# Kernel tuning notes

Hardware: AMD Instinct MI355X
Metric: run time of the kernel (lower is better)

Reference implementation:

```python
import jax, jax.numpy as jnp
import numpy as np

N = 1048576   # total nodes across batch
B = 128       # number of graphs
H = 128       # hidden_size
NEG_SLOPE = 0.01  # LeakyReLU default


def setup_inputs() -> dict:
    key = jax.random.key(0)
    k1, k2, k3, k4 = jax.random.split(key, 4)
    h = jax.random.normal(k1, (N, H), dtype=jnp.float32)
    attention_query = jax.random.normal(k2, (B, H), dtype=jnp.float32)
    w = jax.random.normal(k3, (2 * H,), dtype=jnp.float32) * (1.0 / np.sqrt(2 * H))
    segment_ids = jnp.sort(jax.random.randint(k4, (N,), 0, B, dtype=jnp.int32))
    return {"h": h, "attention_query": attention_query, "w": w, "segment_ids": segment_ids}


def reference(h, attention_query, w, segment_ids):
    # gate_nn(concat([h, q_rep])) = h @ w[:H] + q[seg] @ w[H:], then LeakyReLU
    w_h, w_q = w[:H], w[H:]
    q_score = attention_query @ w_q                      # [B]
    gate = h @ w_h + q_score[segment_ids]                # [N]
    gate = jnp.where(gate >= 0, gate, NEG_SLOPE * gate)  # LeakyReLU
    # segment softmax over nodes of each graph
    m = jax.ops.segment_max(gate, segment_ids, num_segments=B)   # [B]
    m = jnp.where(jnp.isfinite(m), m, 0.0)               # guard empty segments
    e = jnp.exp(gate - m[segment_ids])                   # [N]
    denom = jax.ops.segment_sum(e, segment_ids, num_segments=B)  # [B]
    alpha = e / jnp.maximum(denom, 1e-20)[segment_ids]   # [N]
    # feat_nn takes first half of concat => just h; weighted segment sum
    pooled = jax.ops.segment_sum(alpha[:, None] * h, segment_ids, num_segments=B)  # [B, H]
    return pooled
```

## Files before the change

kernel.cpp:

```cpp
#include <hip/hip_runtime.h>
#include <math.h>

#define N_ROWS 1048576
#define H 128
#define B 128
#define NEG_SLOPE 0.01f

#define GRID_MAIN 2048
#define ROWS_PB (N_ROWS / GRID_MAIN)
#define MAXP 256

__device__ __forceinline__ float dot4(float4 a, float4 b) {
    return a.x * b.x + a.y * b.y + a.z * b.z + a.w * b.w;
}

__global__ __launch_bounds__(256) void qs_init_kernel(const float* __restrict__ aq,
                                                      const float* __restrict__ w,
                                                      float* __restrict__ qs,
                                                      int* __restrict__ counter) {
    if (blockIdx.x == 0 && threadIdx.x < B) counter[threadIdx.x] = 0;
    const int lane = threadIdx.x & 63;
    const int wave = threadIdx.x >> 6;
    const int half = lane >> 5;
    const int hl   = lane & 31;
    const int b    = blockIdx.x * 8 + wave * 2 + half;
    float4 w4 = ((const float4*)(w + H))[hl];
    float4 a4 = ((const float4*)(aq + (long)b * H))[hl];
    float d = dot4(a4, w4);
    #pragma unroll
    for (int off = 1; off < 32; off <<= 1) d += __shfl_xor(d, off, 32);
    if (hl == 0) qs[b] = d;
}

__global__ __launch_bounds__(256) void main_kernel(const float* __restrict__ h,
                                                   const int* __restrict__ seg,
                                                   const float* __restrict__ w,
                                                   const float* __restrict__ qs,
                                                   int* __restrict__ counter,
                                                   float* __restrict__ pm,
                                                   float* __restrict__ pd,
                                                   float* __restrict__ pacc) {
    __shared__ float qs_s[B];
    if (threadIdx.x < B) qs_s[threadIdx.x] = qs[threadIdx.x];
    __syncthreads();

    const int lane = threadIdx.x & 63;
    const int wave = threadIdx.x >> 6;
    const int half = lane >> 5;
    const int hl   = lane & 31;
    const int hwid = wave * 2 + half;
    const long r0  = (long)blockIdx.x * ROWS_PB;

    float4 w4 = ((const float4*)w)[hl];

    const int sFirst = seg[r0];
    const int sLast  = seg[r0 + ROWS_PB - 1];

    if (sFirst == sLast) {
        const float qsv = qs_s[sFirst];
        float  m_run = -1e30f;
        float  d_run = 0.0f;
        float4 acc   = {0.0f, 0.0f, 0.0f, 0.0f};

        for (int it = 0; it < ROWS_PB / 32; ++it) {
            long base = r0 + (long)it * 32 + hwid * 4;
            const float4* hp = (const float4*)(h + base * H) + hl;
            float4 h0 = hp[0];
            float4 h1 = hp[32];
            float4 h2 = hp[64];
            float4 h3 = hp[96];

            float d0 = dot4(h0, w4), d1 = dot4(h1, w4);
            float d2 = dot4(h2, w4), d3 = dot4(h3, w4);

            float s0 = d0 + __shfl_xor(d0, 16, 32);
            float s1 = d1 + __shfl_xor(d1, 16, 32);
            float s2 = d2 + __shfl_xor(d2, 16, 32);
            float s3 = d3 + __shfl_xor(d3, 16, 32);
            float z01 = (hl & 16) ? s1 : s0;
            float z23 = (hl & 16) ? s3 : s2;
            float t01 = z01 + __shfl_xor(z01, 8, 32);
            float t23 = z23 + __shfl_xor(z23, 8, 32);
            float zz  = (hl & 8) ? t23 : t01;
            zz += __shfl_xor(zz, 4, 32);
            zz += __shfl_xor(zz, 2, 32);
            zz += __shfl_xor(zz, 1, 32);
            float g0 = __shfl(zz,  0, 32) + qsv;
            float g1 = __shfl(zz, 16, 32) + qsv;
            float g2 = __shfl(zz,  8, 32) + qsv;
            float g3 = __shfl(zz, 24, 32) + qsv;
            g0 = (g0 >= 0.0f) ? g0 : NEG_SLOPE * g0;
            g1 = (g1 >= 0.0f) ? g1 : NEG_SLOPE * g1;
            g2 = (g2 >= 0.0f) ? g2 : NEG_SLOPE * g2;
            g3 = (g3 >= 0.0f) ? g3 : NEG_SLOPE * g3;

            #pragma unroll
            for (int u = 0; u < 4; ++u) {
                float  g  = (u == 0) ? g0 : (u == 1) ? g1 : (u == 2) ? g2 : g3;
                float4 hv = (u == 0) ? h0 : (u == 1) ? h1 : (u == 2) ? h2 : h3;
                if (g <= m_run) {
                    float e = __expf(g - m_run);
                    acc.x += e * hv.x;
                    acc.y += e * hv.y;
                    acc.z += e * hv.z;
                    acc.w += e * hv.w;
                    d_run += e;
                } else {
                    float sc = __expf(m_run - g);
                    acc.x = acc.x * sc + hv.x;
                    acc.y = acc.y * sc + hv.y;
                    acc.z = acc.z * sc + hv.z;
                    acc.w = acc.w * sc + hv.w;
                    d_run = d_run * sc + 1.0f;
                    m_run = g;
                }
            }
        }
        float m_o = __shfl_xor(m_run, 32);
        float d_o = __shfl_xor(d_run, 32);
        float4 a_o;
        a_o.x = __shfl_xor(acc.x, 32);
        a_o.y = __shfl_xor(acc.y, 32);
        a_o.z = __shfl_xor(acc.z, 32);
        a_o.w = __shfl_xor(acc.w, 32);
        float M  = fmaxf(m_run, m_o);
        float ss = __expf(m_run - M);
        float so = __expf(m_o  - M);
        float4 am;
        am.x = acc.x * ss + a_o.x * so;
        am.y = acc.y * ss + a_o.y * so;
        am.z = acc.z * ss + a_o.z * so;
        am.w = acc.w * ss + a_o.w * so;
        float Dm = d_run * ss + d_o * so;

        int slot = 0;
        if (lane == 0) slot = atomicAdd(counter + sFirst, 1);
        slot = min(__shfl(slot, 0), MAXP - 1);
        long pbase = (long)sFirst * MAXP + slot;
        if (half == 0) ((float4*)(pacc + pbase * H))[hl] = am;
        if (lane == 0) { pm[pbase] = M; pd[pbase] = Dm; }
    } else {
        int    cur   = -1;
        float  m_run = -1e30f;
        float  d_run = 0.0f;
        float4 acc   = {0.0f, 0.0f, 0.0f, 0.0f};

        for (int it = 0; it < ROWS_PB / 16; ++it) {
            long r1 = r0 + hwid + (long)it * 16;
            long r2 = r1 + 8;
            float4 ha = ((const float4*)(h + r1 * H))[hl];
            float4 hb = ((const float4*)(h + r2 * H))[hl];
            int s1 = seg[r1];
            int s2 = seg[r2];

            #pragma unroll
            for (int k = 0; k < 2; ++k) {
                float4 h4 = k ? hb : ha;
                int    s  = k ? s2 : s1;
                float d = dot4(h4, w4);
                #pragma unroll
                for (int off = 1; off < 32; off <<= 1) d += __shfl_xor(d, off, 32);
                float g = d + qs_s[s];
                g = (g >= 0.0f) ? g : NEG_SLOPE * g;

                if (s != cur) {
                    if (cur >= 0) {
                        int slot = 0;
                        if (hl == 0) slot = atomicAdd(counter + cur, 1);
                        slot = min(__shfl(slot, 0, 32), MAXP - 1);
                        long pbase = (long)cur * MAXP + slot;
                        ((float4*)(pacc + pbase * H))[hl] = acc;
                        if (hl == 0) { pm[pbase] = m_run; pd[pbase] = d_run; }
                    }
                    cur = s;
                    m_run = -1e30f;
                    d_run = 0.0f;
                    acc = make_float4(0.0f, 0.0f, 0.0f, 0.0f);
                }
                if (g <= m_run) {
                    float e = __expf(g - m_run);
                    acc.x += e * h4.x;
                    acc.y += e * h4.y;
                    acc.z += e * h4.z;
                    acc.w += e * h4.w;
                    d_run += e;
                } else {
                    float sc = __expf(m_run - g);
                    acc.x = acc.x * sc + h4.x;
                    acc.y = acc.y * sc + h4.y;
                    acc.z = acc.z * sc + h4.z;
                    acc.w = acc.w * sc + h4.w;
                    d_run = d_run * sc + 1.0f;
                    m_run = g;
                }
            }
        }
        if (cur >= 0) {
            int slot = 0;
            if (hl == 0) slot = atomicAdd(counter + cur, 1);
            slot = min(__shfl(slot, 0, 32), MAXP - 1);
            long pbase = (long)cur * MAXP + slot;
            ((float4*)(pacc + pbase * H))[hl] = acc;
            if (hl == 0) { pm[pbase] = m_run; pd[pbase] = d_run; }
        }
    }
}

__global__ __launch_bounds__(128) void merge_kernel(const int* __restrict__ counter,
                                                    const float* __restrict__ pm,
                                                    const float* __restrict__ pd,
                                                    const float* __restrict__ pacc,
                                                    float* __restrict__ out) {
    const int s = blockIdx.x;
    const int t = threadIdx.x;
    const int c = min(counter[s], MAXP);
    const long sb = (long)s * MAXP;

    __shared__ float red[2];
    __shared__ float scv[MAXP];

    float lm = -1e30f;
    for (int j = t; j < c; j += 128) lm = fmaxf(lm, pm[sb + j]);
    #pragma unroll
    for (int off = 1; off < 64; off <<= 1) lm = fmaxf(lm, __shfl_xor(lm, off));
    if ((t & 63) == 0) red[t >> 6] = lm;
    __syncthreads();
    float M = fmaxf(red[0], red[1]);
    __syncthreads();

    float ld = 0.0f;
    for (int j = t; j < c; j += 128) {
        float sc = __expf(pm[sb + j] - M);
        scv[j] = sc;
        ld += pd[sb + j] * sc;
    }
    #pragma unroll
    for (int off = 1; off < 64; off <<= 1) ld += __shfl_xor(ld, off);
    if ((t & 63) == 0) red[t >> 6] = ld;
    __syncthreads();
    float D = red[0] + red[1];

    float a = 0.0f;
    #pragma unroll 4
    for (int j = 0; j < c; ++j) a += pacc[(sb + j) * H + t] * scv[j];

    out[s * H + t] = (c > 0) ? a / fmaxf(D, 1e-20f) : 0.0f;
}

extern "C" void kernel_launch(void* const* d_in, const int* in_sizes, int n_in,
                              void* d_out, int out_size, void* d_ws, size_t ws_size,
                              hipStream_t stream) {
    const float* h   = (const float*)d_in[0];
    const float* aq  = (const float*)d_in[1];
    const float* w   = (const float*)d_in[2];
    const int*   seg = (const int*)d_in[3];
    float* out = (float*)d_out;

    float* ws      = (float*)d_ws;
    float* qs      = ws;
    int*   counter = (int*)(ws + B);
    float* pm      = ws + 2 * B;
    float* pd      = ws + 2 * B + B * MAXP;
    float* pacc    = ws + 2 * B + 2 * B * MAXP;

    qs_init_kernel<<<16, 256, 0, stream>>>(aq, w, qs, counter);
    main_kernel<<<GRID_MAIN, 256, 0, stream>>>(h, seg, w, qs, counter, pm, pd, pacc);
    merge_kernel<<<B, 128, 0, stream>>>(counter, pm, pd, pacc, out);
}
```

Baseline: 701.3 us.

## Batch online-softmax update per 4 rows and merge wave partials in shared memory

```diff
diff --git a/kernel.cpp b/kernel.cpp
--- a/kernel.cpp
+++ b/kernel.cpp
@@ -41,6 +41,9 @@
                                                    float* __restrict__ pd,
                                                    float* __restrict__ pacc) {
     __shared__ float qs_s[B];
+    __shared__ float sm[4];
+    __shared__ float sd[4];
+    __shared__ float sacc[4][H];
     if (threadIdx.x < B) qs_s[threadIdx.x] = qs[threadIdx.x];
     __syncthreads();
 
@@ -94,27 +97,18 @@
             g2 = (g2 >= 0.0f) ? g2 : NEG_SLOPE * g2;
             g3 = (g3 >= 0.0f) ? g3 : NEG_SLOPE * g3;
 
-            #pragma unroll
-            for (int u = 0; u < 4; ++u) {
-                float  g  = (u == 0) ? g0 : (u == 1) ? g1 : (u == 2) ? g2 : g3;
-                float4 hv = (u == 0) ? h0 : (u == 1) ? h1 : (u == 2) ? h2 : h3;
-                if (g <= m_run) {
-                    float e = __expf(g - m_run);
-                    acc.x += e * hv.x;
-                    acc.y += e * hv.y;
-                    acc.z += e * hv.z;
-                    acc.w += e * hv.w;
-                    d_run += e;
-                } else {
-                    float sc = __expf(m_run - g);
-                    acc.x = acc.x * sc + hv.x;
-                    acc.y = acc.y * sc + hv.y;
-                    acc.z = acc.z * sc + hv.z;
-                    acc.w = acc.w * sc + hv.w;
-                    d_run = d_run * sc + 1.0f;
-                    m_run = g;
-                }
-            }
+            float M  = fmaxf(fmaxf(m_run, g0), fmaxf(fmaxf(g1, g2), g3));
+            float sc = __expf(m_run - M);
+            float e0 = __expf(g0 - M);
+            float e1 = __expf(g1 - M);
+            float e2 = __expf(g2 - M);
+            float e3 = __expf(g3 - M);
+            acc.x = fmaf(acc.x, sc, fmaf(e0, h0.x, e1 * h1.x) + fmaf(e2, h2.x, e3 * h3.x));
+            acc.y = fmaf(acc.y, sc, fmaf(e0, h0.y, e1 * h1.y) + fmaf(e2, h2.y, e3 * h3.y));
+            acc.z = fmaf(acc.z, sc, fmaf(e0, h0.z, e1 * h1.z) + fmaf(e2, h2.z, e3 * h3.z));
+            acc.w = fmaf(acc.w, sc, fmaf(e0, h0.w, e1 * h1.w) + fmaf(e2, h2.w, e3 * h3.w));
+            d_run = fmaf(d_run, sc, (e0 + e1) + (e2 + e3));
+            m_run = M;
         }
         float m_o = __shfl_xor(m_run, 32);
         float d_o = __shfl_xor(d_run, 32);
@@ -133,12 +127,28 @@
         am.w = acc.w * ss + a_o.w * so;
         float Dm = d_run * ss + d_o * so;
 
-        int slot = 0;
-        if (lane == 0) slot = atomicAdd(counter + sFirst, 1);
-        slot = min(__shfl(slot, 0), MAXP - 1);
-        long pbase = (long)sFirst * MAXP + slot;
-        if (half == 0) ((float4*)(pacc + pbase * H))[hl] = am;
-        if (lane == 0) { pm[pbase] = M; pd[pbase] = Dm; }
+        if (half == 0) ((float4*)&sacc[wave][0])[hl] = am;
+        if (lane == 0) { sm[wave] = M; sd[wave] = Dm; }
+        __syncthreads();
+        if (wave == 0) {
+            float Mb = fmaxf(fmaxf(sm[0], sm[1]), fmaxf(sm[2], sm[3]));
+            float e0 = __expf(sm[0] - Mb);
+            float e1 = __expf(sm[1] - Mb);
+            float e2 = __expf(sm[2] - Mb);
+            float e3 = __expf(sm[3] - Mb);
+            int c = lane * 2;
+            float2 a;
+            a.x = fmaf(e0, sacc[0][c],     e1 * sacc[1][c])     + fmaf(e2, sacc[2][c],     e3 * sacc[3][c]);
+            a.y = fmaf(e0, sacc[0][c + 1], e1 * sacc[1][c + 1]) + fmaf(e2, sacc[2][c + 1], e3 * sacc[3][c + 1]);
+            float Db = fmaf(e0, sd[0], e1 * sd[1]) + fmaf(e2, sd[2], e3 * sd[3]);
+
+            int slot = 0;
+            if (lane == 0) slot = atomicAdd(counter + sFirst, 1);
+            slot = min(__shfl(slot, 0), MAXP - 1);
+            long pbase = (long)sFirst * MAXP + slot;
+            ((float2*)(pacc + pbase * H))[lane] = a;
+            if (lane == 0) { pm[pbase] = Mb; pd[pbase] = Db; }
+        }
     } else {
         int    cur   = -1;
         float  m_run = -1e30f;
```

Measured after the change: 696.1 us. About the same (-0.7%).
